# Kernel optimization log

Measured on AMD Instinct MI355X. Metric: run time of the kernel, lower is better.

Reference implementation:

```python
import jax, jax.numpy as jnp
import numpy as np

LAM = 0.3          # margin weight lam (halved inside, as in the torch code)
IGNORE = 255       # ignore_index
NEG = -1e30        # finite -inf stand-in for masking the label class


def setup_inputs() -> dict:
    key = jax.random.key(0)
    k1, k2 = jax.random.split(key)
    logits = jax.random.normal(k1, (8, 19, 512, 512), dtype=jnp.float32)
    labels = jax.random.randint(k2, (8, 512, 512), 0, 19)  # no ignored pixels
    return {"logits": logits, "labels": labels}


def _loss_per_pixel(logits, lb):
    # logits: (N, C, H, W) float32, lb: (N, H, W) int in [0, C)
    C = logits.shape[1]
    coeff = 1.0 / (C - 1.0)
    lam = LAM / 2.0
    onehot = jax.nn.one_hot(lb, C, axis=1, dtype=jnp.bool_)  # (N, C, H, W)
    # softmax over the C-1 non-label classes == softmax with label class masked out
    m_logits = jnp.where(onehot, NEG, logits)
    log_q = jax.nn.log_softmax(m_logits, axis=1)
    q = jnp.exp(log_q)
    margin = jnp.where(onehot, 0.0, (q - coeff) * log_q).sum(axis=1) * lam  # (N, H, W)
    # standard cross-entropy term: -log_softmax(logits)[label]
    log_p = jax.nn.log_softmax(logits, axis=1)
    ce = -jnp.take_along_axis(log_p, lb[:, None], axis=1)[:, 0]  # (N, H, W)
    return margin + ce


def reference(logits, labels):
    valid = labels != IGNORE
    lb = jnp.where(valid, labels, 0)
    loss = _loss_per_pixel(logits.astype(jnp.float32), lb)
    vf = valid.astype(loss.dtype)
    # reduction='mean' over non-ignored pixels
    return (loss * vf).sum() / vf.sum()
```

## Files before the change

### kernel.cpp

```cpp
#include <hip/hip_runtime.h>

#define NCLS 19
#define HW (512 * 512)
#define NPIX (8 * HW)
#define NBLK 2048

__global__ __launch_bounds__(256) void lms_main_kernel(
    const float* __restrict__ logits, const int* __restrict__ labels,
    float* __restrict__ partials) {
  const float COEFF = 1.0f / 18.0f;
  const float LAM_HALF = 0.15f;

  int t = blockIdx.x * blockDim.x + threadIdx.x;
  long p = (long)t * 4;

  int n = (int)(p >> 18);
  int hw = (int)(p & (HW - 1));
  const float* base = logits + (size_t)n * NCLS * HW + hw;

  int4 lb4 = *(const int4*)(labels + p);
  int l0 = (lb4.x != 255) ? lb4.x : 0;
  int l1 = (lb4.y != 255) ? lb4.y : 0;
  int l2 = (lb4.z != 255) ? lb4.z : 0;
  int l3 = (lb4.w != 255) ? lb4.w : 0;

  float xl0 = base[(size_t)l0 * HW + 0];
  float xl1 = base[(size_t)l1 * HW + 1];
  float xl2 = base[(size_t)l2 * HW + 2];
  float xl3 = base[(size_t)l3 * HW + 3];

  float s0 = 0.f, s1 = 0.f, s2 = 0.f, s3 = 0.f;
  float T0 = 0.f, T1 = 0.f, T2 = 0.f, T3 = 0.f;
  float S0 = 0.f, S1 = 0.f, S2 = 0.f, S3 = 0.f;
#pragma unroll
  for (int c = 0; c < NCLS; ++c) {
    float4 v = *(const float4*)(base + (size_t)c * HW);
    float e;
    e = __expf(v.x); s0 += e; T0 += e * v.x; S0 += v.x;
    e = __expf(v.y); s1 += e; T1 += e * v.y; S1 += v.y;
    e = __expf(v.z); s2 += e; T2 += e * v.z; S2 += v.z;
    e = __expf(v.w); s3 += e; T3 += e * v.w; S3 += v.w;
  }

  float loss = 0.f, cnt = 0.f;
#define PIXEL(s, T, S, xl, lbv)                                   \
  {                                                               \
    float el = __expf(xl);                                        \
    float sm = s - el;                                            \
    float margin = (T - el * xl) / sm - COEFF * (S - xl);         \
    float ce = __logf(s) - xl;                                    \
    bool valid = (lbv != 255);                                    \
    loss += valid ? (ce + LAM_HALF * margin) : 0.f;               \
    cnt += valid ? 1.f : 0.f;                                     \
  }
  PIXEL(s0, T0, S0, xl0, lb4.x)
  PIXEL(s1, T1, S1, xl1, lb4.y)
  PIXEL(s2, T2, S2, xl2, lb4.z)
  PIXEL(s3, T3, S3, xl3, lb4.w)
#undef PIXEL

#pragma unroll
  for (int off = 32; off > 0; off >>= 1) {
    loss += __shfl_down(loss, off, 64);
    cnt += __shfl_down(cnt, off, 64);
  }

  __shared__ float sl[4], sc[4];
  int wave = threadIdx.x >> 6;
  int lane = threadIdx.x & 63;
  if (lane == 0) {
    sl[wave] = loss;
    sc[wave] = cnt;
  }
  __syncthreads();
  if (threadIdx.x == 0) {
    partials[2 * blockIdx.x] = sl[0] + sl[1] + sl[2] + sl[3];
    partials[2 * blockIdx.x + 1] = sc[0] + sc[1] + sc[2] + sc[3];
  }
}

__global__ __launch_bounds__(1024) void lms_final_kernel(
    const float* __restrict__ partials, float* __restrict__ out) {
  int t = threadIdx.x;
  float loss = partials[2 * t] + partials[2 * (t + 1024)];
  float cnt = partials[2 * t + 1] + partials[2 * (t + 1024) + 1];
#pragma unroll
  for (int off = 32; off > 0; off >>= 1) {
    loss += __shfl_down(loss, off, 64);
    cnt += __shfl_down(cnt, off, 64);
  }
  __shared__ float sl[16], sc[16];
  int wave = t >> 6;
  int lane = t & 63;
  if (lane == 0) {
    sl[wave] = loss;
    sc[wave] = cnt;
  }
  __syncthreads();
  if (t == 0) {
    float L = 0.f, C = 0.f;
#pragma unroll
    for (int w = 0; w < 16; ++w) {
      L += sl[w];
      C += sc[w];
    }
    out[0] = L / C;
  }
}

extern "C" void kernel_launch(void* const* d_in, const int* in_sizes, int n_in,
                              void* d_out, int out_size, void* d_ws, size_t ws_size,
                              hipStream_t stream) {
  const float* logits = (const float*)d_in[0];
  const int* labels = (const int*)d_in[1];
  float* out = (float*)d_out;
  float* partials = (float*)d_ws;

  lms_main_kernel<<<NBLK, 256, 0, stream>>>(logits, labels, partials);
  lms_final_kernel<<<1, 1024, 0, stream>>>(partials, out);
}
```

Before: 228.0 us.

## Stage logits tile into LDS via async global_load_lds, drop label gather

Each block now stages a 19x512 logits tile into shared memory with global_load_lds direct-to-LDS loads. After a barrier, threads compute two pixels each from LDS and read the label-class logit from LDS instead of doing a scattered global gather. This doubles the block count and changes the final reduction to sum four partials per thread. The cost is about 38KB of LDS per block, which caps occupancy, plus a full barrier before any compute, so load and compute no longer overlap within a block.

```diff
diff --git a/kernel.cpp b/kernel.cpp
--- a/kernel.cpp
+++ b/kernel.cpp
@@ -3,7 +3,9 @@
 #define NCLS 19
 #define HW (512 * 512)
 #define NPIX (8 * HW)
-#define NBLK 2048
+#define TILE 512
+#define NBLK (NPIX / TILE)
+#define CHUNKS (NCLS * TILE / 4)
 
 __global__ __launch_bounds__(256) void lms_main_kernel(
     const float* __restrict__ logits, const int* __restrict__ labels,
@@ -11,52 +13,57 @@
   const float COEFF = 1.0f / 18.0f;
   const float LAM_HALF = 0.15f;
 
-  int t = blockIdx.x * blockDim.x + threadIdx.x;
-  long p = (long)t * 4;
+  __shared__ float tile[NCLS * TILE];
 
-  int n = (int)(p >> 18);
-  int hw = (int)(p & (HW - 1));
-  const float* base = logits + (size_t)n * NCLS * HW + hw;
+  const int t = threadIdx.x;
+  const long pixel0 = (long)blockIdx.x * TILE;
+  const int n = (int)(pixel0 >> 18);
+  const int hw0 = (int)(pixel0 & (HW - 1));
+  const float* gbase = logits + (size_t)n * NCLS * HW + hw0;
 
-  int4 lb4 = *(const int4*)(labels + p);
-  int l0 = (lb4.x != 255) ? lb4.x : 0;
-  int l1 = (lb4.y != 255) ? lb4.y : 0;
-  int l2 = (lb4.z != 255) ? lb4.z : 0;
-  int l3 = (lb4.w != 255) ? lb4.w : 0;
+#pragma unroll
+  for (int f = t; f < CHUNKS; f += 256) {
+    int r = f >> 7;
+    int col = f & 127;
+    const float* g = gbase + (size_t)r * HW + col * 4;
+    const __attribute__((address_space(1))) float* g1 =
+        (const __attribute__((address_space(1))) float*)(uintptr_t)g;
+    __attribute__((address_space(3))) float* l3 =
+        (__attribute__((address_space(3))) float*)(uintptr_t)(&tile[f * 4]);
+    __builtin_amdgcn_global_load_lds(g1, l3, 16, 0, 0);
+  }
 
-  float xl0 = base[(size_t)l0 * HW + 0];
-  float xl1 = base[(size_t)l1 * HW + 1];
-  float xl2 = base[(size_t)l2 * HW + 2];
-  float xl3 = base[(size_t)l3 * HW + 3];
+  int2 lb2 = *(const int2*)(labels + pixel0 + 2 * t);
+  int l0 = (lb2.x != 255) ? lb2.x : 0;
+  int l1 = (lb2.y != 255) ? lb2.y : 0;
 
-  float s0 = 0.f, s1 = 0.f, s2 = 0.f, s3 = 0.f;
-  float T0 = 0.f, T1 = 0.f, T2 = 0.f, T3 = 0.f;
-  float S0 = 0.f, S1 = 0.f, S2 = 0.f, S3 = 0.f;
+  __syncthreads();
+
+  float s0 = 0.f, T0 = 0.f, S0 = 0.f;
+  float s1 = 0.f, T1 = 0.f, S1 = 0.f;
 #pragma unroll
   for (int c = 0; c < NCLS; ++c) {
-    float4 v = *(const float4*)(base + (size_t)c * HW);
+    float2 v = *(const float2*)&tile[c * TILE + 2 * t];
     float e;
     e = __expf(v.x); s0 += e; T0 += e * v.x; S0 += v.x;
     e = __expf(v.y); s1 += e; T1 += e * v.y; S1 += v.y;
-    e = __expf(v.z); s2 += e; T2 += e * v.z; S2 += v.z;
-    e = __expf(v.w); s3 += e; T3 += e * v.w; S3 += v.w;
   }
+  float xl0 = tile[l0 * TILE + 2 * t];
+  float xl1 = tile[l1 * TILE + 2 * t + 1];
 
   float loss = 0.f, cnt = 0.f;
-#define PIXEL(s, T, S, xl, lbv)                                   \
-  {                                                               \
-    float el = __expf(xl);                                        \
-    float sm = s - el;                                            \
-    float margin = (T - el * xl) / sm - COEFF * (S - xl);         \
-    float ce = __logf(s) - xl;                                    \
-    bool valid = (lbv != 255);                                    \
-    loss += valid ? (ce + LAM_HALF * margin) : 0.f;               \
-    cnt += valid ? 1.f : 0.f;                                     \
+#define PIXEL(s, T, S, xl, lbv)                           \
+  {                                                       \
+    float el = __expf(xl);                                \
+    float sm = s - el;                                    \
+    float margin = (T - el * xl) / sm - COEFF * (S - xl); \
+    float ce = __logf(s) - xl;                            \
+    bool valid = (lbv != 255);                            \
+    loss += valid ? (ce + LAM_HALF * margin) : 0.f;       \
+    cnt += valid ? 1.f : 0.f;                             \
   }
-  PIXEL(s0, T0, S0, xl0, lb4.x)
-  PIXEL(s1, T1, S1, xl1, lb4.y)
-  PIXEL(s2, T2, S2, xl2, lb4.z)
-  PIXEL(s3, T3, S3, xl3, lb4.w)
+  PIXEL(s0, T0, S0, xl0, lb2.x)
+  PIXEL(s1, T1, S1, xl1, lb2.y)
 #undef PIXEL
 
 #pragma unroll
@@ -64,16 +71,15 @@
     loss += __shfl_down(loss, off, 64);
     cnt += __shfl_down(cnt, off, 64);
   }
-
   __shared__ float sl[4], sc[4];
-  int wave = threadIdx.x >> 6;
-  int lane = threadIdx.x & 63;
+  int wave = t >> 6;
+  int lane = t & 63;
   if (lane == 0) {
     sl[wave] = loss;
     sc[wave] = cnt;
   }
   __syncthreads();
-  if (threadIdx.x == 0) {
+  if (t == 0) {
     partials[2 * blockIdx.x] = sl[0] + sl[1] + sl[2] + sl[3];
     partials[2 * blockIdx.x + 1] = sc[0] + sc[1] + sc[2] + sc[3];
   }
@@ -82,8 +88,13 @@
 __global__ __launch_bounds__(1024) void lms_final_kernel(
     const float* __restrict__ partials, float* __restrict__ out) {
   int t = threadIdx.x;
-  float loss = partials[2 * t] + partials[2 * (t + 1024)];
-  float cnt = partials[2 * t + 1] + partials[2 * (t + 1024) + 1];
+  float loss = 0.f, cnt = 0.f;
+#pragma unroll
+  for (int k = 0; k < 4; ++k) {
+    float2 pr = ((const float2*)partials)[t + 1024 * k];
+    loss += pr.x;
+    cnt += pr.y;
+  }
 #pragma unroll
   for (int off = 32; off > 0; off >>= 1) {
     loss += __shfl_down(loss, off, 64);
```

After: 222.4 us. 1.03x faster.
